# Optimization experiments

Hardware: AMD Instinct MI355X
Metric: run time of the kernel (lower is better)

Reference implementation:

```python
import jax, jax.numpy as jnp
import numpy as np

B, S, T = 32, 64, 48
V, E, H = 32000, 512, 1024
PAD = 0
NEG = jnp.float32(-1e9)


def gru_cell(x, h, wih, whh, bih, bhh):
    # torch nn.GRU gate order: r, z, n
    gi = x @ wih.T + bih            # (B, 3H)
    gh = h @ whh.T + bhh            # (B, 3H)
    ir, iz, inn = jnp.split(gi, 3, axis=1)
    hr, hz, hn = jnp.split(gh, 3, axis=1)
    r = jax.nn.sigmoid(ir + hr)
    z = jax.nn.sigmoid(iz + hz)
    n = jnp.tanh(inn + r * hn)
    return (1.0 - z) * n + z * h


def setup_inputs() -> dict:
    key = jax.random.key(0)
    ks = jax.random.split(key, 32)
    p = lambda k, shp: jax.random.normal(k, shp, jnp.float32) * 0.02
    inp = {}
    inp['src_ids'] = jax.random.randint(ks[0], (B, S), 0, V)
    inp['src_lens'] = jnp.full((B,), S, dtype=jnp.int32)
    inp['tgt_ids'] = jax.random.randint(ks[1], (B, T), 0, V)
    # embeddings, pad row zeroed (padding_idx)
    inp['enc_emb'] = p(ks[2], (V, E)).at[PAD].set(0.0)
    inp['dec_emb'] = p(ks[3], (V, E)).at[PAD].set(0.0)
    # encoder 2-layer GRU
    inp['enc_wih0'] = p(ks[4], (3 * H, E)); inp['enc_whh0'] = p(ks[5], (3 * H, H))
    inp['enc_bih0'] = p(ks[6], (3 * H,));  inp['enc_bhh0'] = p(ks[7], (3 * H,))
    inp['enc_wih1'] = p(ks[8], (3 * H, H)); inp['enc_whh1'] = p(ks[9], (3 * H, H))
    inp['enc_bih1'] = p(ks[10], (3 * H,)); inp['enc_bhh1'] = p(ks[11], (3 * H,))
    # decoder 2-layer GRU, input = emb + context = E + H
    inp['dec_wih0'] = p(ks[12], (3 * H, E + H)); inp['dec_whh0'] = p(ks[13], (3 * H, H))
    inp['dec_bih0'] = p(ks[14], (3 * H,)); inp['dec_bhh0'] = p(ks[15], (3 * H,))
    inp['dec_wih1'] = p(ks[16], (3 * H, H)); inp['dec_whh1'] = p(ks[17], (3 * H, H))
    inp['dec_bih1'] = p(ks[18], (3 * H,)); inp['dec_bhh1'] = p(ks[19], (3 * H,))
    # multiplicative attention and output projection
    inp['attn_w'] = p(ks[20], (H, H))
    inp['out_w'] = p(ks[21], (V, H + H))
    inp['out_b'] = p(ks[22], (V,))
    return inp


def reference(src_ids, src_lens, tgt_ids,
              enc_emb, dec_emb,
              enc_wih0, enc_whh0, enc_bih0, enc_bhh0,
              enc_wih1, enc_whh1, enc_bih1, enc_bhh1,
              dec_wih0, dec_whh0, dec_bih0, dec_bhh0,
              dec_wih1, dec_whh1, dec_bih1, dec_bhh1,
              attn_w, out_w, out_b):
    b = src_ids.shape[0]
    # ---- encoder: 2-layer GRU over source (src_lens are all full -> packing is a no-op)
    emb = enc_emb[src_ids]                              # (B,S,E)
    h0 = jnp.zeros((b, H), emb.dtype)
    h1 = jnp.zeros((b, H), emb.dtype)

    def estep(carry, x_t):
        h0, h1 = carry
        h0 = gru_cell(x_t, h0, enc_wih0, enc_whh0, enc_bih0, enc_bhh0)
        h1 = gru_cell(h0, h1, enc_wih1, enc_whh1, enc_bih1, enc_bhh1)
        return (h0, h1), h1

    (h0, h1), enc_seq = jax.lax.scan(estep, (h0, h1), emb.transpose(1, 0, 2))
    enc_out = enc_seq.transpose(1, 0, 2)                # (B,S,H)

    src_mask = src_ids != PAD                           # (B,S)
    proj = enc_out @ attn_w.T                           # (B,S,H) multiplicative attn W(enc_out)

    # ---- decoder: teacher forcing ratio = 1.0 -> inputs are tgt[:, :-1]
    def dstep(carry, y_t):
        d0, d1 = carry
        e = dec_emb[y_t]                                # (B,E)
        score = jnp.einsum('bsh,bh->bs', proj, d1)
        score = jnp.where(src_mask, score, NEG)
        attn = jax.nn.softmax(score, axis=1)            # (B,S)
        ctx = jnp.einsum('bs,bsh->bh', attn, enc_out)   # (B,H)
        x = jnp.concatenate([e, ctx], axis=1)           # (B,E+H)
        d0 = gru_cell(x, d0, dec_wih0, dec_whh0, dec_bih0, dec_bhh0)
        d1 = gru_cell(d0, d1, dec_wih1, dec_whh1, dec_bih1, dec_bhh1)
        logits = jnp.concatenate([d1, ctx], axis=1) @ out_w.T + out_b  # (B,V)
        return (d0, d1), logits

    _, logits_seq = jax.lax.scan(dstep, (h0, h1), tgt_ids[:, :-1].T)
    return logits_seq.transpose(1, 0, 2)                # (B,T-1,V)
```

## Files before the change

kernel.cpp:

```cpp
#include <hip/hip_runtime.h>
#include <math.h>

#define B_  32
#define S_  64
#define T_  48
#define V_  32000
#define E_  512
#define H_  1024
#define G3  3072

typedef __attribute__((ext_vector_type(8))) short short8;
typedef __attribute__((ext_vector_type(4))) float f32x4;

__device__ __forceinline__ ushort f2bf(float x) {
    unsigned u = __float_as_uint(x);
    return (ushort)((u + 0x7FFF + ((u >> 16) & 1)) >> 16);
}
__device__ __forceinline__ void cvt4(float4 v, ushort4& h, ushort4& l) {
    ushort h0 = f2bf(v.x), h1 = f2bf(v.y), h2 = f2bf(v.z), h3 = f2bf(v.w);
    l.x = f2bf(v.x - __uint_as_float((unsigned)h0 << 16));
    l.y = f2bf(v.y - __uint_as_float((unsigned)h1 << 16));
    l.z = f2bf(v.z - __uint_as_float((unsigned)h2 << 16));
    l.w = f2bf(v.w - __uint_as_float((unsigned)h3 << 16));
    h.x = h0; h.y = h1; h.z = h2; h.w = h3;
}

__global__ __launch_bounds__(256)
void gemm_mfma(const float* __restrict__ A, int lda,
               const int* __restrict__ ids, int id_mode,
               const float* __restrict__ W, int ldw,
               const float* __restrict__ bias,
               float* __restrict__ C, int out_mode, int ldc,
               int M, int K)
{
    __shared__ __align__(16) ushort AhS[128][40];
    __shared__ __align__(16) ushort AlS[128][40];
    __shared__ __align__(16) ushort BhS[128][40];
    __shared__ __align__(16) ushort BlS[128][40];

    const int tid = threadIdx.x;
    const int n0  = blockIdx.x * 128;
    const int m0  = blockIdx.y * 128;
    const int sr  = tid >> 1;
    const int sk  = (tid & 1) * 16;

    long abase;
    {
        int m = m0 + sr;
        if (id_mode == 0) {
            abase = (long)m * lda;
        } else {
            int t = m >> 5, b = m & 31;
            int idx = (id_mode == 1) ? (b * S_ + t) : (b * T_ + t);
            abase = (long)ids[idx] * lda;
        }
    }
    const float* Ar = A + abase + sk;
    const float* Wr = W + (long)(n0 + sr) * ldw + sk;

    const int lane = tid & 63;
    const int wv   = tid >> 6;
    const int wr   = (wv >> 1) * 64;
    const int wc   = (wv & 1) * 64;
    const int lr   = lane & 15;
    const int lk   = (lane >> 4) * 8;

    f32x4 acc[4][4];
    const f32x4 fz = {0.f, 0.f, 0.f, 0.f};
#pragma unroll
    for (int i = 0; i < 4; ++i)
#pragma unroll
        for (int j = 0; j < 4; ++j) acc[i][j] = fz;

    for (int k0 = 0; k0 < K; k0 += 32) {
        float4 a4[4], w4[4];
#pragma unroll
        for (int q = 0; q < 4; ++q) {
            a4[q] = *(const float4*)(Ar + k0 + q * 4);
            w4[q] = *(const float4*)(Wr + k0 + q * 4);
        }
        __syncthreads();
#pragma unroll
        for (int q = 0; q < 4; ++q) {
            ushort4 h, l;
            cvt4(a4[q], h, l);
            *(ushort4*)&AhS[sr][sk + q * 4] = h;
            *(ushort4*)&AlS[sr][sk + q * 4] = l;
            cvt4(w4[q], h, l);
            *(ushort4*)&BhS[sr][sk + q * 4] = h;
            *(ushort4*)&BlS[sr][sk + q * 4] = l;
        }
        __syncthreads();

        short8 fah[4], fbh[4];
#pragma unroll
        for (int i = 0; i < 4; ++i) {
            fah[i] = *(const short8*)&AhS[wr + i * 16 + lr][lk];
            fbh[i] = *(const short8*)&BhS[wc + i * 16 + lr][lk];
        }
#pragma unroll
        for (int i = 0; i < 4; ++i)
#pragma unroll
            for (int j = 0; j < 4; ++j)
                acc[i][j] = __builtin_amdgcn_mfma_f32_16x16x32_bf16(fah[i], fbh[j], acc[i][j], 0, 0, 0);
        {
            short8 fal[4];
#pragma unroll
            for (int i = 0; i < 4; ++i)
                fal[i] = *(const short8*)&AlS[wr + i * 16 + lr][lk];
#pragma unroll
            for (int i = 0; i < 4; ++i)
#pragma unroll
                for (int j = 0; j < 4; ++j)
                    acc[i][j] = __builtin_amdgcn_mfma_f32_16x16x32_bf16(fal[i], fbh[j], acc[i][j], 0, 0, 0);
        }
        {
            short8 fbl[4];
#pragma unroll
            for (int j = 0; j < 4; ++j)
                fbl[j] = *(const short8*)&BlS[wc + j * 16 + lr][lk];
#pragma unroll
            for (int i = 0; i < 4; ++i)
#pragma unroll
                for (int j = 0; j < 4; ++j)
                    acc[i][j] = __builtin_amdgcn_mfma_f32_16x16x32_bf16(fah[i], fbl[j], acc[i][j], 0, 0, 0);
        }
    }

    float bcol[4] = {0.f, 0.f, 0.f, 0.f};
    if (bias) {
#pragma unroll
        for (int j = 0; j < 4; ++j) bcol[j] = bias[n0 + wc + j * 16 + lr];
    }
    const int rbase = (lane >> 4) * 4;
#pragma unroll
    for (int i = 0; i < 4; ++i) {
#pragma unroll
        for (int r = 0; r < 4; ++r) {
            int m = m0 + wr + i * 16 + rbase + r;
            float* crow;
            if (out_mode == 0) {
                crow = C + (long)m * ldc;
            } else {
                if (m >= M) continue;
                int t = m >> 5, b2 = m & 31;
                crow = C + (long)b2 * ((T_ - 1) * V_) + (long)t * V_;
            }
#pragma unroll
            for (int j = 0; j < 4; ++j)
                crow[n0 + wc + j * 16 + lr] = acc[i][j][r] + bcol[j];
        }
    }
}

template<int HAS_X, int HAS_GI>
__global__ __launch_bounds__(256)
void gru_layer(const float* __restrict__ x, int xld,
               const float* __restrict__ wx, int wxld, int wxoff,
               const float* __restrict__ bih,
               const float* __restrict__ gi_pre,
               const float* __restrict__ h,
               const float* __restrict__ whh,
               const float* __restrict__ bhh,
               float* __restrict__ h_new,
               float* __restrict__ seq_out, long seq_stride)
{
    const int j0  = blockIdx.x * 2;
    const int tid = threadIdx.x;
    const int b   = tid & 31;
    const int ks  = tid >> 5;
    __shared__ float redh[2][3][8][32];
    __shared__ float redx[2][3][8][32];

    const float* hr  = h + (long)b * H_;
    const float* wh  = whh + (long)j0 * H_;
    const float* xr  = nullptr;
    const float* wxb = nullptr;
    if (HAS_X) {
        xr  = x + (long)b * xld;
        wxb = wx + (long)j0 * wxld + wxoff;
    }

    float ah[2][3] = {};
    float ax[2][3] = {};
    const int k0 = ks * 128;
#pragma unroll 2
    for (int k = k0; k < k0 + 128; k += 4) {
        float4 hv = *(const float4*)(hr + k);
        float4 xv;
        if (HAS_X) xv = *(const float4*)(xr + k);
#pragma unroll
        for (int u = 0; u < 2; ++u) {
#pragma unroll
            for (int g = 0; g < 3; ++g) {
                float4 wv = *(const float4*)(wh + ((long)g * H_ + u) * H_ + k);
                ah[u][g] += hv.x*wv.x + hv.y*wv.y + hv.z*wv.z + hv.w*wv.w;
                if (HAS_X) {
                    float4 uv = *(const float4*)(wxb + ((long)g * H_ + u) * wxld + k);
                    ax[u][g] += xv.x*uv.x + xv.y*uv.y + xv.z*uv.z + xv.w*uv.w;
                }
            }
        }
    }
#pragma unroll
    for (int u = 0; u < 2; ++u)
#pragma unroll
        for (int g = 0; g < 3; ++g) {
            redh[u][g][ks][b] = ah[u][g];
            if (HAS_X) redx[u][g][ks][b] = ax[u][g];
        }
    __syncthreads();
    if (tid < 64) {
        const int u  = tid >> 5;
        const int bb = tid & 31;
        const int j  = j0 + u;
        float gh0 = bhh[j], gh1 = bhh[H_ + j], gh2 = bhh[2*H_ + j];
#pragma unroll
        for (int q = 0; q < 8; ++q) {
            gh0 += redh[u][0][q][bb]; gh1 += redh[u][1][q][bb]; gh2 += redh[u][2][q][bb];
        }
        float gi0, gi1, gi2;
        if (HAS_GI) {
            const float* g = gi_pre + (long)bb * G3;
            gi0 = g[j]; gi1 = g[H_ + j]; gi2 = g[2*H_ + j];
        } else {
            gi0 = bih[j]; gi1 = bih[H_ + j]; gi2 = bih[2*H_ + j];
        }
        if (HAS_X) {
#pragma unroll
            for (int q = 0; q < 8; ++q) {
                gi0 += redx[u][0][q][bb]; gi1 += redx[u][1][q][bb]; gi2 += redx[u][2][q][bb];
            }
        }
        float r = 1.f / (1.f + expf(-(gi0 + gh0)));
        float z = 1.f / (1.f + expf(-(gi1 + gh1)));
        float n = tanhf(gi2 + r * gh2);
        float hv = h[(long)bb * H_ + j];
        float o = (1.f - z) * n + z * hv;
        h_new[(long)bb * H_ + j] = o;
        if (seq_out) seq_out[(long)bb * seq_stride + j] = o;
    }
}

__global__ __launch_bounds__(256)
void attention_kernel(const float* __restrict__ proj,
                      const float* __restrict__ enc_out,
                      const int* __restrict__ src_ids,
                      const float* __restrict__ d1,
                      float* __restrict__ ctx_out)
{
    const int b = blockIdx.x;
    const int tid = threadIdx.x;
    __shared__ __align__(16) float dl[H_];
    __shared__ float attn[S_];

    *(float4*)&dl[tid * 4] = *(const float4*)(d1 + (long)b * H_ + tid * 4);
    __syncthreads();

    const int lane = tid & 63, wid = tid >> 6;
    for (int s = wid; s < S_; s += 4) {
        const float* pr = proj + ((long)b * S_ + s) * H_;
        float a = 0.f;
#pragma unroll
        for (int c = 0; c < 4; ++c) {
            float4 pv = *(const float4*)(pr + c * 256 + lane * 4);
            float4 dv = *(const float4*)&dl[c * 256 + lane * 4];
            a += pv.x*dv.x + pv.y*dv.y + pv.z*dv.z + pv.w*dv.w;
        }
#pragma unroll
        for (int off = 32; off > 0; off >>= 1) a += __shfl_xor(a, off);
        if (lane == 0) attn[s] = (src_ids[b * S_ + s] != 0) ? a : -1e9f;
    }
    __syncthreads();
    if (tid < 64) {
        float v = attn[tid];
        float mx = v;
#pragma unroll
        for (int off = 32; off > 0; off >>= 1) mx = fmaxf(mx, __shfl_xor(mx, off));
        float e = expf(v - mx);
        float sm = e;
#pragma unroll
        for (int off = 32; off > 0; off >>= 1) sm += __shfl_xor(sm, off);
        attn[tid] = e / sm;
    }
    __syncthreads();
    float4 acc = make_float4(0.f, 0.f, 0.f, 0.f);
    const float* eb = enc_out + (long)b * S_ * H_ + tid * 4;
    for (int s = 0; s < S_; ++s) {
        float w = attn[s];
        float4 ev = *(const float4*)(eb + (long)s * H_);
        acc.x += w * ev.x; acc.y += w * ev.y; acc.z += w * ev.z; acc.w += w * ev.w;
    }
    *(float4*)(ctx_out + (long)b * 2048 + tid * 4) = acc;
}

extern "C" void kernel_launch(void* const* d_in, const int* in_sizes, int n_in,
                              void* d_out, int out_size, void* d_ws, size_t ws_size,
                              hipStream_t stream)
{
    (void)in_sizes; (void)n_in; (void)out_size; (void)ws_size;
    const int*   src_ids  = (const int*)  d_in[0];
    const int*   tgt_ids  = (const int*)  d_in[2];
    const float* enc_emb  = (const float*)d_in[3];
    const float* dec_emb  = (const float*)d_in[4];
    const float* enc_wih0 = (const float*)d_in[5];
    const float* enc_whh0 = (const float*)d_in[6];
    const float* enc_bih0 = (const float*)d_in[7];
    const float* enc_bhh0 = (const float*)d_in[8];
    const float* enc_wih1 = (const float*)d_in[9];
    const float* enc_whh1 = (const float*)d_in[10];
    const float* enc_bih1 = (const float*)d_in[11];
    const float* enc_bhh1 = (const float*)d_in[12];
    const float* dec_wih0 = (const float*)d_in[13];
    const float* dec_whh0 = (const float*)d_in[14];
    const float* dec_bih0 = (const float*)d_in[15];
    const float* dec_bhh0 = (const float*)d_in[16];
    const float* dec_wih1 = (const float*)d_in[17];
    const float* dec_whh1 = (const float*)d_in[18];
    const float* dec_bih1 = (const float*)d_in[19];
    const float* dec_bhh1 = (const float*)d_in[20];
    const float* attn_w   = (const float*)d_in[21];
    const float* out_w    = (const float*)d_in[22];
    const float* out_b    = (const float*)d_in[23];
    float* out = (float*)d_out;

    float* ws      = (float*)d_ws;
    float* gi_enc0 = ws;
    float* gi_dec  = gi_enc0 + 2048L * G3;
    float* enc_out = gi_dec  + 1536L * G3;
    float* proj    = enc_out + 2048L * H_;
    float* cat     = proj    + 2048L * H_;
    float* states  = cat     + 1536L * 2048;
    float* h0[2] = { states,             states + 1L*B_*H_ };
    float* h1[2] = { states + 2L*B_*H_,  states + 3L*B_*H_ };
    float* enc_l0  = cat;

    hipMemsetAsync(states, 0, 4L * B_ * H_ * sizeof(float), stream);

    gemm_mfma<<<dim3(24, 16), 256, 0, stream>>>(enc_emb, E_, src_ids, 1, enc_wih0, E_, enc_bih0,
                                                gi_enc0, 0, G3, 2048, E_);
    gemm_mfma<<<dim3(24, 12), 256, 0, stream>>>(dec_emb, E_, tgt_ids, 2, dec_wih0, E_ + H_, dec_bih0,
                                                gi_dec, 0, G3, 1536, E_);

    int p = 0;
    for (int t = 0; t < S_; ++t) {
        gru_layer<0, 1><<<512, 256, 0, stream>>>(
            nullptr, 0, nullptr, 0, 0, nullptr,
            gi_enc0 + (long)t * B_ * G3, h0[p], enc_whh0, enc_bhh0,
            h0[1 - p], enc_l0 + (long)t * B_ * H_, (long)H_);
        p ^= 1;
    }

    gemm_mfma<<<dim3(24, 16), 256, 0, stream>>>(enc_l0, H_, nullptr, 0, enc_wih1, H_, enc_bih1,
                                                gi_enc0, 0, G3, 2048, H_);

    p = 0;
    for (int t = 0; t < S_; ++t) {
        gru_layer<0, 1><<<512, 256, 0, stream>>>(
            nullptr, 0, nullptr, 0, 0, nullptr,
            gi_enc0 + (long)t * B_ * G3, h1[p], enc_whh1, enc_bhh1,
            h1[1 - p], enc_out + (long)t * H_, (long)S_ * H_);
        p ^= 1;
    }

    gemm_mfma<<<dim3(8, 16), 256, 0, stream>>>(enc_out, H_, nullptr, 0, attn_w, H_, nullptr,
                                               proj, 0, H_, 2048, H_);

    for (int t = 0; t < T_ - 1; ++t) {
        attention_kernel<<<B_, 256, 0, stream>>>(proj, enc_out, src_ids, h1[p],
                                                 cat + (long)t * B_ * 2048 + H_);
        gru_layer<1, 1><<<512, 256, 0, stream>>>(
            cat + (long)t * B_ * 2048 + H_, 2048,
            dec_wih0, E_ + H_, E_,
            nullptr, gi_dec + (long)t * B_ * G3,
            h0[p], dec_whh0, dec_bhh0,
            h0[1 - p], nullptr, 0);
        gru_layer<1, 0><<<512, 256, 0, stream>>>(
            h0[1 - p], H_, dec_wih1, H_, 0, dec_bih1, nullptr,
            h1[p], dec_whh1, dec_bhh1,
            h1[1 - p], cat + (long)t * B_ * 2048, 2048);
        p ^= 1;
    }

    gemm_mfma<<<dim3(V_ / 128, 12), 256, 0, stream>>>(cat, 2048, nullptr, 0, out_w, 2048, out_b,
                                                      out, 1, 0, 1504, 2048);
}
```

Baseline: 9.152 ms.

## Fuse per-timestep GRU and attention launches into persistent kernels with grid barriers

```diff
diff --git a/kernel.cpp b/kernel.cpp
--- a/kernel.cpp
+++ b/kernel.cpp
@@ -23,6 +23,19 @@
     l.z = f2bf(v.z - __uint_as_float((unsigned)h2 << 16));
     l.w = f2bf(v.w - __uint_as_float((unsigned)h3 << 16));
     h.x = h0; h.y = h1; h.z = h2; h.w = h3;
+}
+
+__device__ __forceinline__ void gsync(unsigned* cnt, unsigned nb, unsigned& tgt) {
+    __syncthreads();
+    __builtin_amdgcn_fence(__ATOMIC_RELEASE, "agent");
+    if (threadIdx.x == 0) {
+        __hip_atomic_fetch_add(cnt, 1u, __ATOMIC_RELAXED, __HIP_MEMORY_SCOPE_AGENT);
+        tgt += nb;
+        while (__hip_atomic_load(cnt, __ATOMIC_RELAXED, __HIP_MEMORY_SCOPE_AGENT) < tgt)
+            __builtin_amdgcn_s_sleep(1);
+    }
+    __syncthreads();
+    __builtin_amdgcn_fence(__ATOMIC_ACQUIRE, "agent");
 }
 
 __global__ __launch_bounds__(256)
@@ -154,23 +167,23 @@
 }
 
 template<int HAS_X, int HAS_GI>
-__global__ __launch_bounds__(256)
-void gru_layer(const float* __restrict__ x, int xld,
-               const float* __restrict__ wx, int wxld, int wxoff,
-               const float* __restrict__ bih,
-               const float* __restrict__ gi_pre,
-               const float* __restrict__ h,
-               const float* __restrict__ whh,
-               const float* __restrict__ bhh,
-               float* __restrict__ h_new,
-               float* __restrict__ seq_out, long seq_stride)
+__device__ __forceinline__ void gru_phase(
+    float* sm, int j0,
+    const float* __restrict__ x, int xld,
+    const float* __restrict__ wx, int wxld, int wxoff,
+    const float* __restrict__ bih,
+    const float* __restrict__ gi_pre,
+    const float* __restrict__ h,
+    const float* __restrict__ whh,
+    const float* __restrict__ bhh,
+    float* __restrict__ h_new,
+    float* __restrict__ seq_out, long seq_stride)
 {
-    const int j0  = blockIdx.x * 2;
     const int tid = threadIdx.x;
     const int b   = tid & 31;
     const int ks  = tid >> 5;
-    __shared__ float redh[2][3][8][32];
-    __shared__ float redx[2][3][8][32];
+    float* redh = sm;
+    float* redx = sm + 2 * 3 * 8 * 32;
 
     const float* hr  = h + (long)b * H_;
     const float* wh  = whh + (long)j0 * H_;
@@ -206,8 +219,8 @@
     for (int u = 0; u < 2; ++u)
 #pragma unroll
         for (int g = 0; g < 3; ++g) {
-            redh[u][g][ks][b] = ah[u][g];
-            if (HAS_X) redx[u][g][ks][b] = ax[u][g];
+            redh[((u * 3 + g) * 8 + ks) * 32 + b] = ah[u][g];
+            if (HAS_X) redx[((u * 3 + g) * 8 + ks) * 32 + b] = ax[u][g];
         }
     __syncthreads();
     if (tid < 64) {
@@ -217,7 +230,9 @@
         float gh0 = bhh[j], gh1 = bhh[H_ + j], gh2 = bhh[2*H_ + j];
 #pragma unroll
         for (int q = 0; q < 8; ++q) {
-            gh0 += redh[u][0][q][bb]; gh1 += redh[u][1][q][bb]; gh2 += redh[u][2][q][bb];
+            gh0 += redh[((u * 3 + 0) * 8 + q) * 32 + bb];
+            gh1 += redh[((u * 3 + 1) * 8 + q) * 32 + bb];
+            gh2 += redh[((u * 3 + 2) * 8 + q) * 32 + bb];
         }
         float gi0, gi1, gi2;
         if (HAS_GI) {
@@ -229,7 +244,9 @@
         if (HAS_X) {
 #pragma unroll
             for (int q = 0; q < 8; ++q) {
-                gi0 += redx[u][0][q][bb]; gi1 += redx[u][1][q][bb]; gi2 += redx[u][2][q][bb];
+                gi0 += redx[((u * 3 + 0) * 8 + q) * 32 + bb];
+                gi1 += redx[((u * 3 + 1) * 8 + q) * 32 + bb];
+                gi2 += redx[((u * 3 + 2) * 8 + q) * 32 + bb];
             }
         }
         float r = 1.f / (1.f + expf(-(gi0 + gh0)));
@@ -242,56 +259,110 @@
     }
 }
 
-__global__ __launch_bounds__(256)
-void attention_kernel(const float* __restrict__ proj,
-                      const float* __restrict__ enc_out,
-                      const int* __restrict__ src_ids,
-                      const float* __restrict__ d1,
-                      float* __restrict__ ctx_out)
+__global__ __launch_bounds__(256, 2)
+void enc_loop(const float* __restrict__ gi, const float* __restrict__ whh,
+              const float* __restrict__ bhh,
+              float* __restrict__ ha, float* __restrict__ hb,
+              float* __restrict__ seq, long t_stride, long b_stride, int T,
+              unsigned* cnt)
 {
-    const int b = blockIdx.x;
-    const int tid = threadIdx.x;
-    __shared__ __align__(16) float dl[H_];
-    __shared__ float attn[S_];
-
-    *(float4*)&dl[tid * 4] = *(const float4*)(d1 + (long)b * H_ + tid * 4);
-    __syncthreads();
-
-    const int lane = tid & 63, wid = tid >> 6;
-    for (int s = wid; s < S_; s += 4) {
-        const float* pr = proj + ((long)b * S_ + s) * H_;
-        float a = 0.f;
-#pragma unroll
-        for (int c = 0; c < 4; ++c) {
-            float4 pv = *(const float4*)(pr + c * 256 + lane * 4);
-            float4 dv = *(const float4*)&dl[c * 256 + lane * 4];
-            a += pv.x*dv.x + pv.y*dv.y + pv.z*dv.z + pv.w*dv.w;
-        }
-#pragma unroll
-        for (int off = 32; off > 0; off >>= 1) a += __shfl_xor(a, off);
-        if (lane == 0) attn[s] = (src_ids[b * S_ + s] != 0) ? a : -1e9f;
-    }
-    __syncthreads();
-    if (tid < 64) {
-        float v = attn[tid];
-        float mx = v;
-#pragma unroll
-        for (int off = 32; off > 0; off >>= 1) mx = fmaxf(mx, __shfl_xor(mx, off));
-        float e = expf(v - mx);
-        float sm = e;
-#pragma unroll
-        for (int off = 32; off > 0; off >>= 1) sm += __shfl_xor(sm, off);
-        attn[tid] = e / sm;
-    }
-    __syncthreads();
-    float4 acc = make_float4(0.f, 0.f, 0.f, 0.f);
-    const float* eb = enc_out + (long)b * S_ * H_ + tid * 4;
-    for (int s = 0; s < S_; ++s) {
-        float w = attn[s];
-        float4 ev = *(const float4*)(eb + (long)s * H_);
-        acc.x += w * ev.x; acc.y += w * ev.y; acc.z += w * ev.z; acc.w += w * ev.w;
-    }
-    *(float4*)(ctx_out + (long)b * 2048 + tid * 4) = acc;
+    __shared__ float sm[2 * 3 * 8 * 32];
+    const int j0 = blockIdx.x * 2;
+    float* h[2] = { ha, hb };
+    unsigned tgt = 0;
+    int p = 0;
+    for (int t = 0; t < T; ++t) {
+        gru_phase<0, 1>(sm, j0, nullptr, 0, nullptr, 0, 0, nullptr,
+                        gi + (long)t * B_ * G3,
+                        h[p], whh, bhh, h[1 - p],
+                        seq + (long)t * t_stride, b_stride);
+        gsync(cnt, 512, tgt);
+        p ^= 1;
+    }
+}
+
+__global__ __launch_bounds__(256, 2)
+void dec_loop(const float* __restrict__ proj, const float* __restrict__ enc_out,
+              const int* __restrict__ src_ids, const float* __restrict__ gi_dec,
+              const float* __restrict__ wih0, const float* __restrict__ whh0,
+              const float* __restrict__ bhh0,
+              const float* __restrict__ wih1, const float* __restrict__ bih1,
+              const float* __restrict__ whh1, const float* __restrict__ bhh1,
+              float* __restrict__ cat,
+              float* __restrict__ h0a, float* __restrict__ h0b,
+              float* __restrict__ h1a, float* __restrict__ h1b,
+              float* __restrict__ scores, unsigned* cnt)
+{
+    __shared__ float sm[2 * 2 * 3 * 8 * 32];
+    __shared__ float at[S_];
+    __shared__ float red4[4][64];
+    float* h0[2] = { h0a, h0b };
+    float* h1[2] = { h1a, h1b };
+    const int blk = blockIdx.x, tid = threadIdx.x;
+    unsigned tgt = 0;
+    int p = 0;
+    for (int t = 0; t < T_ - 1; ++t) {
+        {
+            const int b    = blk >> 4;
+            const int s    = ((blk & 15) << 2) + (tid >> 6);
+            const int lane = tid & 63;
+            const float* pr = proj + ((long)b * S_ + s) * H_;
+            const float* dr = h1[p] + (long)b * H_;
+            float a = 0.f;
+#pragma unroll
+            for (int c = 0; c < 4; ++c) {
+                float4 pv = *(const float4*)(pr + c * 256 + lane * 4);
+                float4 dv = *(const float4*)(dr + c * 256 + lane * 4);
+                a += pv.x*dv.x + pv.y*dv.y + pv.z*dv.z + pv.w*dv.w;
+            }
+#pragma unroll
+            for (int off = 32; off > 0; off >>= 1) a += __shfl_xor(a, off);
+            if (lane == 0)
+                scores[b * S_ + s] = (src_ids[b * S_ + s] != 0) ? a : -1e9f;
+        }
+        gsync(cnt, 512, tgt);
+        {
+            const int b  = blk >> 4;
+            const int hs = (blk & 15) * 64;
+            if (tid < 64) {
+                float v = scores[b * S_ + tid];
+                float mx = v;
+#pragma unroll
+                for (int off = 32; off > 0; off >>= 1) mx = fmaxf(mx, __shfl_xor(mx, off));
+                float e = expf(v - mx);
+                float smm = e;
+#pragma unroll
+                for (int off = 32; off > 0; off >>= 1) smm += __shfl_xor(smm, off);
+                at[tid] = e / smm;
+            }
+            __syncthreads();
+            const int h  = hs + (tid & 63);
+            const int sg = tid >> 6;
+            const float* eb = enc_out + (long)b * S_ * H_ + h;
+            float a = 0.f;
+            for (int s = sg * 16; s < sg * 16 + 16; ++s)
+                a += at[s] * eb[(long)s * H_];
+            red4[sg][tid & 63] = a;
+            __syncthreads();
+            if (tid < 64)
+                cat[(long)t * B_ * 2048 + (long)b * 2048 + H_ + hs + tid] =
+                    red4[0][tid] + red4[1][tid] + red4[2][tid] + red4[3][tid];
+        }
+        gsync(cnt, 512, tgt);
+        gru_phase<1, 1>(sm, blk * 2,
+                        cat + (long)t * B_ * 2048 + H_, 2048,
+                        wih0, E_ + H_, E_, nullptr,
+                        gi_dec + (long)t * B_ * G3,
+                        h0[p], whh0, bhh0, h0[1 - p], nullptr, 0);
+        gsync(cnt, 512, tgt);
+        gru_phase<1, 0>(sm, blk * 2,
+                        h0[1 - p], H_,
+                        wih1, H_, 0, bih1, nullptr,
+                        h1[p], whh1, bhh1, h1[1 - p],
+                        cat + (long)t * B_ * 2048, 2048);
+        gsync(cnt, 512, tgt);
+        p ^= 1;
+    }
 }
 
 extern "C" void kernel_launch(void* const* d_in, const int* in_sizes, int n_in,
@@ -331,56 +402,37 @@
     float* proj    = enc_out + 2048L * H_;
     float* cat     = proj    + 2048L * H_;
     float* states  = cat     + 1536L * 2048;
-    float* h0[2] = { states,             states + 1L*B_*H_ };
-    float* h1[2] = { states + 2L*B_*H_,  states + 3L*B_*H_ };
+    unsigned* cnts = (unsigned*)(states + 4L * B_ * H_);
+    float* scores  = (float*)(cnts + 64);
+    float* h0a = states;
+    float* h0b = states + 1L * B_ * H_;
+    float* h1a = states + 2L * B_ * H_;
+    float* h1b = states + 3L * B_ * H_;
     float* enc_l0  = cat;
 
-    hipMemsetAsync(states, 0, 4L * B_ * H_ * sizeof(float), stream);
+    hipMemsetAsync(states, 0, (4L * B_ * H_ + 64) * sizeof(float), stream);
 
     gemm_mfma<<<dim3(24, 16), 256, 0, stream>>>(enc_emb, E_, src_ids, 1, enc_wih0, E_, enc_bih0,
                                                 gi_enc0, 0, G3, 2048, E_);
     gemm_mfma<<<dim3(24, 12), 256, 0, stream>>>(dec_emb, E_, tgt_ids, 2, dec_wih0, E_ + H_, dec_bih0,
                                                 gi_dec, 0, G3, 1536, E_);
 
-    int p = 0;
-    for (int t = 0; t < S_; ++t) {
-        gru_layer<0, 1><<<512, 256, 0, stream>>>(
-            nullptr, 0, nullptr, 0, 0, nullptr,
-            gi_enc0 + (long)t * B_ * G3, h0[p], enc_whh0, enc_bhh0,
-            h0[1 - p], enc_l0 + (long)t * B_ * H_, (long)H_);
-        p ^= 1;
-    }
+    enc_loop<<<512, 256, 0, stream>>>(gi_enc0, enc_whh0, enc_bhh0, h0a, h0b,
+                                      enc_l0, (long)B_ * H_, (long)H_, S_, cnts + 0);
 
     gemm_mfma<<<dim3(24, 16), 256, 0, stream>>>(enc_l0, H_, nullptr, 0, enc_wih1, H_, enc_bih1,
                                                 gi_enc0, 0, G3, 2048, H_);
 
-    p = 0;
-    for (int t = 0; t < S_; ++t) {
-        gru_layer<0, 1><<<512, 256, 0, stream>>>(
-            nullptr, 0, nullptr, 0, 0, nullptr,
-            gi_enc0 + (long)t * B_ * G3, h1[p], enc_whh1, enc_bhh1,
-            h1[1 - p], enc_out + (long)t * H_, (long)S_ * H_);
-        p ^= 1;
-    }
+    enc_loop<<<512, 256, 0, stream>>>(gi_enc0, enc_whh1, enc_bhh1, h1a, h1b,
+                                      enc_out, (long)H_, (long)S_ * H_, S_, cnts + 16);
 
     gemm_mfma<<<dim3(8, 16), 256, 0, stream>>>(enc_out, H_, nullptr, 0, attn_w, H_, nullptr,
                                                proj, 0, H_, 2048, H_);
 
-    for (int t = 0; t < T_ - 1; ++t) {
-        attention_kernel<<<B_, 256, 0, stream>>>(proj, enc_out, src_ids, h1[p],
-                                                 cat + (long)t * B_ * 2048 + H_);
-        gru_layer<1, 1><<<512, 256, 0, stream>>>(
-            cat + (long)t * B_ * 2048 + H_, 2048,
-            dec_wih0, E_ + H_, E_,
-            nullptr, gi_dec + (long)t * B_ * G3,
-            h0[p], dec_whh0, dec_bhh0,
-            h0[1 - p], nullptr, 0);
-        gru_layer<1, 0><<<512, 256, 0, stream>>>(
-            h0[1 - p], H_, dec_wih1, H_, 0, dec_bih1, nullptr,
-            h1[p], dec_whh1, dec_bhh1,
-            h1[1 - p], cat + (long)t * B_ * 2048, 2048);
-        p ^= 1;
-    }
+    dec_loop<<<512, 256, 0, stream>>>(proj, enc_out, src_ids, gi_dec,
+                                      dec_wih0, dec_whh0, dec_bhh0,
+                                      dec_wih1, dec_bih1, dec_whh1, dec_bhh1,
+                                      cat, h0a, h0b, h1a, h1b, scores, cnts + 32);
 
     gemm_mfma<<<dim3(V_ / 128, 12), 256, 0, stream>>>(cat, 2048, nullptr, 0, out_w, 2048, out_b,
                                                       out, 1, 0, 1504, 2048);
```

Measured after the change: 31.44 ms. 244% more time.
